# Kernel optimization log

Measured on AMD Instinct MI355X. Metric: run time of the kernel, lower is better.

Reference implementation:

```python
import jax, jax.numpy as jnp
import numpy as np

EPS = 1e-5

def setup_inputs() -> dict:
    key = jax.random.key(0)
    ks = jax.random.split(key, 6)
    N, E, C, H, L = 50000, 800000, 128, 128, 3
    x = jax.random.normal(ks[0], (N, C), dtype=jnp.float32)
    edge_index = jax.random.randint(ks[1], (2, E), 0, N, dtype=jnp.int64)
    # Xavier-ish scaled weights; layer 0 uses in=C=H so all layers stack uniformly.
    Wl = jax.random.normal(ks[2], (L, C, H), dtype=jnp.float32) / np.sqrt(C)
    Wr = jax.random.normal(ks[3], (L, C, H), dtype=jnp.float32) / np.sqrt(C)
    b = jnp.zeros((L, H), dtype=jnp.float32)
    gamma = jnp.ones((L, H), dtype=jnp.float32)
    beta = jnp.zeros((L, H), dtype=jnp.float32)
    return {"x": x, "edge_index": edge_index, "Wl": Wl, "Wr": Wr, "b": b,
            "gamma": gamma, "beta": beta}

def _sage_bn_relu(x, src, dst, Wl, Wr, b, gamma, beta):
    N = x.shape[0]
    # mean aggregation of source features into target nodes (PyG SAGEConv default)
    agg = jax.ops.segment_sum(x[src], dst, num_segments=N)          # [N, C]
    deg = jax.ops.segment_sum(jnp.ones_like(dst, dtype=x.dtype), dst, num_segments=N)
    mean_nbr = agg / jnp.maximum(deg, 1.0)[:, None]
    h = mean_nbr @ Wl + x @ Wr + b                                   # [N, H]
    # BatchNorm1d (training-mode batch statistics over nodes)
    mu = jnp.mean(h, axis=0)
    var = jnp.var(h, axis=0)
    h = gamma * (h - mu) * jax.lax.rsqrt(var + EPS) + beta
    return jax.nn.relu(h)  # dropout omitted (deterministic reference, p->0)

def reference(x, edge_index, Wl, Wr, b, gamma, beta):
    src, dst = edge_index[0], edge_index[1]
    h = x
    for l in range(Wl.shape[0]):
        h = _sage_bn_relu(h, src, dst, Wl[l], Wr[l], b[l], gamma[l], beta[l])
    return h
```

## Files before the change

kernel.cpp:

```cpp
#include <hip/hip_runtime.h>
#include <hip/hip_bf16.h>

#define BN_EPS 1e-5f
#define NPASS 4
#define NKEY 512
#define BCAP2 6144

typedef unsigned short u16;
typedef unsigned int u32;
typedef __attribute__((ext_vector_type(8))) short bf16x8v;
typedef __attribute__((ext_vector_type(4))) float f32x4v;

__device__ __forceinline__ float bf2f(u16 u){
    union { u32 i; float f; } c; c.i = ((u32)u) << 16; return c.f;
}
__device__ __forceinline__ u16 f2bf(float f){
    union { float f; u32 i; } c; c.f = f;
    u32 x = c.i;
    u32 r = x + 0x7FFFu + ((x >> 16) & 1u);
    return (u16)(r >> 16);
}
__device__ __forceinline__ float lo16(u32 u){
    union { u32 i; float f; } c; c.i = u << 16; return c.f;
}
__device__ __forceinline__ float hi16(u32 u){
    union { u32 i; float f; } c; c.i = u & 0xFFFF0000u; return c.f;
}
__device__ __forceinline__ u32 pack2(float f0, float f1){
    return (u32)f2bf(f0) | ((u32)f2bf(f1) << 16);
}

__global__ void detect_k(const int* __restrict__ ei, const u16* __restrict__ xu,
                         int* __restrict__ flags){
    int lane = threadIdx.x;
    unsigned long long bal = __ballot(ei[2 * lane + 1] != 0);
    int cnt = 0;
    #pragma unroll
    for (int k = 0; k < 4; ++k){
        u16 u = xu[2 * (lane + 64 * k)];
        int e = (u >> 7) & 0xFF;
        cnt += (e >= 0x70 && e <= 0x86) ? 1 : 0;
    }
    #pragma unroll
    for (int off = 1; off < 64; off <<= 1) cnt += __shfl_xor(cnt, off);
    if (lane == 0){
        flags[0] = (bal == 0ULL) ? 1 : 0;
        flags[1] = (cnt >= 128) ? 1 : 0;
    }
}

__global__ void prep_k(const void* __restrict__ x, const void* __restrict__ Wl,
                       const void* __restrict__ Wr, const void* __restrict__ b,
                       const void* __restrict__ g, const void* __restrict__ be,
                       u16* __restrict__ xb, u16* __restrict__ wT, float* __restrict__ p,
                       int total4, int wtot, int per, const int* __restrict__ flags){
    int i = blockIdx.x * blockDim.x + threadIdx.x;
    int bf = flags[1];
    if (i < total4){
        if (bf){
            ((uint2*)xb)[i] = ((const uint2*)x)[i];
        } else {
            float4 v = ((const float4*)x)[i];
            ushort4 o; o.x = f2bf(v.x); o.y = f2bf(v.y); o.z = f2bf(v.z); o.w = f2bf(v.w);
            ((ushort4*)xb)[i] = o;
        }
    }
    if (i < wtot){
        u16 vl = bf ? ((const u16*)Wl)[i] : f2bf(((const float*)Wl)[i]);
        u16 vr = bf ? ((const u16*)Wr)[i] : f2bf(((const float*)Wr)[i]);
        int l = i >> 14, r = (i >> 7) & 127, c = i & 127;
        wT[(size_t)(l * 2 + 0) * 16384 + c * 128 + r] = vl;
        wT[(size_t)(l * 2 + 1) * 16384 + c * 128 + r] = vr;
    }
    if (i < per){
        if (bf){
            p[i]           = bf2f(((const u16*)b)[i]);
            p[per + i]     = bf2f(((const u16*)g)[i]);
            p[2 * per + i] = bf2f(((const u16*)be)[i]);
        } else {
            p[i]           = ((const float*)b)[i];
            p[per + i]     = ((const float*)g)[i];
            p[2 * per + i] = ((const float*)be)[i];
        }
    }
}

__global__ __launch_bounds__(1024) void phist_k(const void* __restrict__ ei, int E,
                                                int tile, u32* __restrict__ blockHist,
                                                const int* __restrict__ flags){
    __shared__ u32 lh[NKEY];
    int tid = threadIdx.x;
    if (tid < NKEY) lh[tid] = 0u;
    __syncthreads();
    int start = blockIdx.x * tile;
    int end = min(E, start + tile);
    int i64 = flags[0];
    for (int i = start + tid; i < end; i += 1024){
        int s, d;
        if (i64){
            const long long* p = (const long long*)ei;
            s = (int)p[i]; d = (int)p[E + i];
        } else {
            const int* p = (const int*)ei;
            s = p[i]; d = p[E + i];
        }
        int key = ((s >> 14) << 7) | (d >> 9);
        atomicAdd(&lh[key], 1u);
    }
    __syncthreads();
    if (tid < NKEY) blockHist[blockIdx.x * NKEY + tid] = lh[tid];
}

__global__ __launch_bounds__(512) void bases_k(const u32* __restrict__ blockHist,
                                               u32* __restrict__ blockBase,
                                               int* __restrict__ rangeBase,
                                               int* __restrict__ rp2N, int nb){
    __shared__ u32 t_s[NKEY];
    int k = threadIdx.x;
    u32 run = 0;
    #pragma unroll 8
    for (int b = 0; b < nb; ++b){
        blockBase[b * NKEY + k] = run;
        run += blockHist[b * NKEY + k];
    }
    t_s[k] = min(run, (u32)BCAP2);
    __syncthreads();
    if (k == 0){
        u32 r = 0;
        for (int j = 0; j < NKEY; ++j){ u32 v = t_s[j]; t_s[j] = r; r += v; }
        rangeBase[NKEY] = (int)r;
        *rp2N = (int)r;
    }
    __syncthreads();
    rangeBase[k] = (int)t_s[k];
}

__global__ __launch_bounds__(1024) void pscat_k(const void* __restrict__ ei, int E,
                                                int tile, const u32* __restrict__ blockBase,
                                                u32* __restrict__ part,
                                                const int* __restrict__ flags){
    __shared__ u32 lcur[NKEY];
    int tid = threadIdx.x;
    if (tid < NKEY) lcur[tid] = blockBase[blockIdx.x * NKEY + tid];
    __syncthreads();
    int start = blockIdx.x * tile;
    int end = min(E, start + tile);
    int i64 = flags[0];
    for (int i = start + tid; i < end; i += 1024){
        int s, d;
        if (i64){
            const long long* p = (const long long*)ei;
            s = (int)p[i]; d = (int)p[E + i];
        } else {
            const int* p = (const int*)ei;
            s = p[i]; d = p[E + i];
        }
        int key = ((s >> 14) << 7) | (d >> 9);
        u32 pos = atomicAdd(&lcur[key], 1u);
        if (pos < BCAP2) part[(size_t)key * BCAP2 + pos] = (u32)(u16)s | ((u32)(d & 511) << 16);
    }
}

__global__ __launch_bounds__(1024) void build_k(const u32* __restrict__ part,
                                                const int* __restrict__ rangeBase,
                                                int* __restrict__ rowptr2,
                                                u16* __restrict__ col, int N){
    __shared__ u32 bins[512];
    __shared__ u32 wsum[8];
    __shared__ u16 sorted[BCAP2];
    int key  = blockIdx.x;
    int tid  = threadIdx.x;
    int base = rangeBase[key];
    int cntk = rangeBase[key + 1] - base;
    int p    = key >> 7;
    int d0   = (key & 127) << 9;
    if (tid < 512) bins[tid] = 0u;
    __syncthreads();
    const u32* pk = part + (size_t)key * BCAP2;
    for (int i = tid; i < cntk; i += 1024)
        atomicAdd(&bins[pk[i] >> 16], 1u);
    __syncthreads();
    int lane = tid & 63, w = tid >> 6;
    u32 v = (tid < 512) ? bins[tid] : 0u;
    u32 sc = v;
    #pragma unroll
    for (int off = 1; off < 64; off <<= 1){
        u32 u = __shfl_up(sc, off);
        if (lane >= off) sc += u;
    }
    if (lane == 63 && w < 8) wsum[w] = sc;
    __syncthreads();
    if (tid == 0){
        u32 r = 0;
        #pragma unroll
        for (int j = 0; j < 8; ++j){ u32 t = wsum[j]; wsum[j] = r; r += t; }
    }
    __syncthreads();
    u32 excl = (w < 8 ? wsum[w] : 0u) + sc - v;
    if (tid < 512){
        int d = d0 + tid;
        if (d < N) rowptr2[(size_t)p * N + d] = base + (int)excl;
        bins[tid] = excl;
    }
    __syncthreads();
    for (int i = tid; i < cntk; i += 1024){
        u32 e = pk[i];
        u32 pos = atomicAdd(&bins[e >> 16], 1u);
        sorted[pos] = (u16)e;
    }
    __syncthreads();
    for (int i = tid; i < cntk; i += 1024)
        col[base + i] = sorted[i];
}

#define ACC8(A, G) \
    A[0] += lo16(G.x); A[1] += hi16(G.x); \
    A[2] += lo16(G.y); A[3] += hi16(G.y); \
    A[4] += lo16(G.z); A[5] += hi16(G.z); \
    A[6] += lo16(G.w); A[7] += hi16(G.w);

__global__ __launch_bounds__(256) void agg_k(const u16* __restrict__ h,
                                             const int* __restrict__ rp2,
                                             const u16* __restrict__ col,
                                             u16* __restrict__ meanb, int N){
    int tid  = threadIdx.x;
    int gwid = (blockIdx.x * 256 + tid) >> 6;
    int lane = tid & 63;
    int quad = lane >> 4;
    int sub  = lane & 15;
    if (gwid * 8 >= N) return;
    int d0 = gwid * 8 + quad * 2;
    int d1 = d0 + 1;

    float a0[8] = {0.f,0.f,0.f,0.f,0.f,0.f,0.f,0.f};
    float a1[8] = {0.f,0.f,0.f,0.f,0.f,0.f,0.f,0.f};
    int g0 = 0, g1 = 0;

    for (int p = 0; p < NPASS; ++p){
        const int* rp = rp2 + (size_t)p * N;
        int s0 = 0, e0 = 0, s1 = 0, e1 = 0;
        if (d0 < N){ s0 = rp[d0]; e0 = rp[d0 + 1]; }
        if (d1 < N){ s1 = rp[d1]; e1 = rp[d1 + 1]; }
        g0 += e0 - s0; g1 += e1 - s1;
        int i0 = s0, i1 = s1;
        for (; i0 + 1 < e0 && i1 + 1 < e1; i0 += 2, i1 += 2){
            int sa = col[i0], sb = col[i0 + 1], sc = col[i1], sd = col[i1 + 1];
            uint4 ga = *(const uint4*)(h + (size_t)sa * 128 + sub * 8);
            uint4 gb = *(const uint4*)(h + (size_t)sb * 128 + sub * 8);
            uint4 gc = *(const uint4*)(h + (size_t)sc * 128 + sub * 8);
            uint4 gd = *(const uint4*)(h + (size_t)sd * 128 + sub * 8);
            ACC8(a0, ga); ACC8(a0, gb);
            ACC8(a1, gc); ACC8(a1, gd);
        }
        for (; i0 + 1 < e0; i0 += 2){
            int sa = col[i0], sb = col[i0 + 1];
            uint4 ga = *(const uint4*)(h + (size_t)sa * 128 + sub * 8);
            uint4 gb = *(const uint4*)(h + (size_t)sb * 128 + sub * 8);
            ACC8(a0, ga); ACC8(a0, gb);
        }
        if (i0 < e0){
            int sa = col[i0];
            uint4 ga = *(const uint4*)(h + (size_t)sa * 128 + sub * 8);
            ACC8(a0, ga);
        }
        for (; i1 + 1 < e1; i1 += 2){
            int sc = col[i1], sd = col[i1 + 1];
            uint4 gc = *(const uint4*)(h + (size_t)sc * 128 + sub * 8);
            uint4 gd = *(const uint4*)(h + (size_t)sd * 128 + sub * 8);
            ACC8(a1, gc); ACC8(a1, gd);
        }
        if (i1 < e1){
            int sc = col[i1];
            uint4 gc = *(const uint4*)(h + (size_t)sc * 128 + sub * 8);
            ACC8(a1, gc);
        }
    }

    if (d0 < N){
        float di = 1.f / fmaxf((float)g0, 1.f);
        uint4 o;
        o.x = pack2(a0[0] * di, a0[1] * di);
        o.y = pack2(a0[2] * di, a0[3] * di);
        o.z = pack2(a0[4] * di, a0[5] * di);
        o.w = pack2(a0[6] * di, a0[7] * di);
        *(uint4*)(meanb + (size_t)d0 * 128 + sub * 8) = o;
    }
    if (d1 < N){
        float di = 1.f / fmaxf((float)g1, 1.f);
        uint4 o;
        o.x = pack2(a1[0] * di, a1[1] * di);
        o.y = pack2(a1[2] * di, a1[3] * di);
        o.z = pack2(a1[4] * di, a1[5] * di);
        o.w = pack2(a1[6] * di, a1[7] * di);
        *(uint4*)(meanb + (size_t)d1 * 128 + sub * 8) = o;
    }
}
#undef ACC8

__global__ __launch_bounds__(256, 2) void gemm_k(
        const u16* __restrict__ Aa, const u16* __restrict__ Ab,
        const u16* __restrict__ wT, const float* __restrict__ bias,
        float* __restrict__ stats, u16* __restrict__ hp16, int N, int NT){
    __shared__ __align__(16) u16 sA[16384];
    int tid  = threadIdx.x;
    int lane = tid & 63;
    int w    = tid >> 6;
    int hl   = lane & 15;
    int quad = lane >> 4;
    int c0   = (2 * w)     * 16 + hl;
    int c1   = (2 * w + 1) * 16 + hl;

    bf16x8v Bf[2][2][4];
    {
        const u16* bp = wT + (size_t)(2 * w) * 2048 + (size_t)hl * 128 + quad * 8;
        #pragma unroll
        for (int tl = 0; tl < 2; ++tl)
            #pragma unroll
            for (int half = 0; half < 2; ++half)
                #pragma unroll
                for (int kc = 0; kc < 4; ++kc)
                    Bf[tl][half][kc] =
                        *(const bf16x8v*)(bp + tl * 2048 + half * 16384 + kc * 32);
    }
    float bv0 = bias[c0], bv1 = bias[c1];
    float cs0 = 0.f, cq0 = 0.f, cs1 = 0.f, cq1 = 0.f;

    int smat[4], srow[4], ssub[4], sldo[4];
    #pragma unroll
    for (int i = 0; i < 4; ++i){
        int kk  = w * 4 + i;
        int off = (kk & 7) * 1024 + lane * 16;
        int mat = kk >> 3;
        int row = off >> 8;
        int sub = (off >> 4) & 15;
        smat[i] = mat; srow[i] = row; ssub[i] = sub;
        sldo[i] = mat * 4096 + row * 128 + ((sub ^ (row & 7)) * 8);
    }
    uint4 rg0, rg1, rg2, rg3;

#define STAGE_REGS(T) { \
    int m0_ = (T) * 32; \
    int rb0_ = m0_;      if (rb0_ + 16 > N) rb0_ = N - 16; \
    int rb1_ = m0_ + 16; if (rb1_ + 16 > N) rb1_ = N - 16; \
    _Pragma("unroll") \
    for (int i_ = 0; i_ < 4; ++i_){ \
        int row_  = srow[i_]; \
        int grow_ = (row_ < 16) ? (rb0_ + row_) : (rb1_ + row_ - 16); \
        const u16* src_ = (smat[i_] ? Ab : Aa) + (size_t)grow_ * 128 + ssub[i_] * 8; \
        uint4 v_ = *(const uint4*)src_; \
        if (i_ == 0) rg0 = v_; else if (i_ == 1) rg1 = v_; \
        else if (i_ == 2) rg2 = v_; else rg3 = v_; \
    } }

#define STAGE_WRITE(B) { \
    u16* bb_ = sA + (B) * 8192; \
    *(uint4*)(bb_ + sldo[0]) = rg0; \
    *(uint4*)(bb_ + sldo[1]) = rg1; \
    *(uint4*)(bb_ + sldo[2]) = rg2; \
    *(uint4*)(bb_ + sldo[3]) = rg3; }

#define COMPUTE(B, T) { \
    int m0_ = (T) * 32; \
    int rb0_ = m0_;      bool v0_ = (m0_ + 16 <= N); if (!v0_) rb0_ = N - 16; \
    int rb1_ = m0_ + 16; bool v1_ = (m0_ + 32 <= N); if (!v1_) rb1_ = N - 16; \
    const u16* base_ = sA + (B) * 8192; \
    bf16x8v Af[2][2][4];    \
    _Pragma("unroll") \
    for (int kc_ = 0; kc_ < 4; ++kc_){ \
        int sl_ = ((quad + kc_ * 4) ^ (hl & 7)) * 8; \
        Af[0][0][kc_] = *(const bf16x8v*)(base_ +        hl * 128        + sl_); \
        Af[1][0][kc_] = *(const bf16x8v*)(base_ + (16 + hl) * 128        + sl_); \
        Af[0][1][kc_] = *(const bf16x8v*)(base_ + 4096 +        hl * 128 + sl_); \
        Af[1][1][kc_] = *(const bf16x8v*)(base_ + 4096 + (16 + hl) * 128 + sl_); \
    } \
    f32x4v acc0_[2], acc1_[2]; \
    acc0_[0] = (f32x4v){0.f,0.f,0.f,0.f}; acc0_[1] = (f32x4v){0.f,0.f,0.f,0.f}; \
    acc1_[0] = (f32x4v){0.f,0.f,0.f,0.f}; acc1_[1] = (f32x4v){0.f,0.f,0.f,0.f}; \
    _Pragma("unroll") \
    for (int half_ = 0; half_ < 2; ++half_) \
        _Pragma("unroll") \
        for (int kc_ = 0; kc_ < 4; ++kc_) \
            _Pragma("unroll") \
            for (int tl_ = 0; tl_ < 2; ++tl_){ \
                acc0_[tl_] = __builtin_amdgcn_mfma_f32_16x16x32_bf16( \
                    Af[0][half_][kc_], Bf[tl_][half_][kc_], acc0_[tl_], 0, 0, 0); \
                acc1_[tl_] = __builtin_amdgcn_mfma_f32_16x16x32_bf16( \
                    Af[1][half_][kc_], Bf[tl_][half_][kc_], acc1_[tl_], 0, 0, 0); \
            } \
    _Pragma("unroll") \
    for (int tl_ = 0; tl_ < 2; ++tl_){ \
        int   c_  = tl_ ? c1 : c0; \
        float bv_ = tl_ ? bv1 : bv0; \
        if (v0_){ \
            _Pragma("unroll") \
            for (int r_ = 0; r_ < 4; ++r_){ \
                float vv_ = acc0_[tl_][r_] + bv_; \
                hp16[(size_t)(rb0_ + quad * 4 + r_) * 128 + c_] = f2bf(vv_); \
                if (tl_){ cs1 += vv_; cq1 += vv_ * vv_; } else { cs0 += vv_; cq0 += vv_ * vv_; } \
            } \
        } \
        if (v1_){ \
            _Pragma("unroll") \
            for (int r_ = 0; r_ < 4; ++r_){ \
                float vv_ = acc1_[tl_][r_] + bv_; \
                hp16[(size_t)(rb1_ + quad * 4 + r_) * 128 + c_] = f2bf(vv_); \
                if (tl_){ cs1 += vv_; cq1 += vv_ * vv_; } else { cs0 += vv_; cq0 += vv_ * vv_; } \
            } \
        } \
    } }

    int t = blockIdx.x;
    int G = gridDim.x;
    int cur = 0;
    STAGE_REGS(t);
    STAGE_WRITE(0);
    __syncthreads();
    for (;;){
        int tn = t + G;
        bool hN = (tn < NT);
        if (hN) STAGE_REGS(tn);
        COMPUTE(cur, t);
        if (!hN) break;
        STAGE_WRITE(cur ^ 1);
        __syncthreads();
        cur ^= 1;
        t = tn;
    }
#undef STAGE_REGS
#undef STAGE_WRITE
#undef COMPUTE

    cs0 += __shfl_xor(cs0, 16); cs0 += __shfl_xor(cs0, 32);
    cq0 += __shfl_xor(cq0, 16); cq0 += __shfl_xor(cq0, 32);
    cs1 += __shfl_xor(cs1, 16); cs1 += __shfl_xor(cs1, 32);
    cq1 += __shfl_xor(cq1, 16); cq1 += __shfl_xor(cq1, 32);
    if (quad == 0){
        float* st = stats + (size_t)(blockIdx.x & 63) * 256;
        atomicAdd(&st[c0],       cs0);
        atomicAdd(&st[128 + c0], cq0);
        atomicAdd(&st[c1],       cs1);
        atomicAdd(&st[128 + c1], cq1);
    }
}

__global__ __launch_bounds__(256) void apply_k(
        const u16* __restrict__ in, const float* __restrict__ stats,
        const float* __restrict__ g, const float* __restrict__ be,
        u16* __restrict__ outb, float* __restrict__ outf, int use_f32,
        int total4, float invN){
    __shared__ float s_red[256];
    __shared__ float s_ss[256];
    int tid = threadIdx.x;
    float s = 0.f;
    #pragma unroll 8
    for (int bkt = 0; bkt < 64; ++bkt) s += stats[bkt * 256 + tid];
    s_red[tid] = s;
    __syncthreads();
    if (tid < 128){
        float mu  = s_red[tid] * invN;
        float var = s_red[128 + tid] * invN - mu * mu;
        if (!(mu == mu)) mu = 0.f;
        if (!(var >= 0.f) || !(var == var)) var = 0.f;
        float sc = g[tid] * rsqrtf(var + BN_EPS);
        s_ss[tid]       = sc;
        s_ss[128 + tid] = be[tid] - mu * sc;
    }
    __syncthreads();
    int c = (tid & 31) * 4;
    float sc0 = s_ss[c],     sh0 = s_ss[128 + c];
    float sc1 = s_ss[c + 1], sh1 = s_ss[129 + c];
    float sc2 = s_ss[c + 2], sh2 = s_ss[130 + c];
    float sc3 = s_ss[c + 3], sh3 = s_ss[131 + c];
    for (int i = blockIdx.x * blockDim.x + tid; i < total4; i += blockDim.x * gridDim.x){
        uint2 u = ((const uint2*)in)[i];
        float4 v;
        v.x = lo16(u.x); v.y = hi16(u.x); v.z = lo16(u.y); v.w = hi16(u.y);
        if (!(v.x == v.x)) v.x = 0.f;
        if (!(v.y == v.y)) v.y = 0.f;
        if (!(v.z == v.z)) v.z = 0.f;
        if (!(v.w == v.w)) v.w = 0.f;
        float r0 = fmaxf(v.x * sc0 + sh0, 0.f);
        float r1 = fmaxf(v.y * sc1 + sh1, 0.f);
        float r2 = fmaxf(v.z * sc2 + sh2, 0.f);
        float r3 = fmaxf(v.w * sc3 + sh3, 0.f);
        if (use_f32){
            float4 o; o.x = r0; o.y = r1; o.z = r2; o.w = r3;
            ((float4*)outf)[i] = o;
        } else {
            uint2 o; o.x = pack2(r0, r1); o.y = pack2(r2, r3);
            ((uint2*)outb)[i] = o;
        }
    }
}

extern "C" void kernel_launch(void* const* d_in, const int* in_sizes, int n_in,
                              void* d_out, int out_size, void* d_ws, size_t ws_size,
                              hipStream_t stream){
    const void* x  = d_in[0];
    const int*  ei = (const int*)d_in[1];
    const void* Wl = d_in[2];
    const void* Wr = d_in[3];
    const void* b  = d_in[4];
    const void* gm = d_in[5];
    const void* bt = d_in[6];
    float* outf = (float*)d_out;

    const int N = in_sizes[0] / 128;
    const int E = in_sizes[1] / 2;
    const int L = in_sizes[2] / 16384;
    const int PB = 128;
    const int TILE = (E + PB - 1) / PB;

    char* wsp = (char*)d_ws;
    size_t off = 0;
    auto alloc = [&](size_t bytes) -> char* {
        char* p = wsp + off;
        off = (off + bytes + 255) & ~(size_t)255;
        return p;
    };
    int*   flags  = (int*)  alloc(16);
    int*   rowptr2= (int*)  alloc(((size_t)NPASS * N + 1) * 4);
    u16*   col    = (u16*)  alloc((size_t)E * 2);
    u32*   bHist  = (u32*)  alloc((size_t)PB * NKEY * 4);
    u32*   bBase  = (u32*)  alloc((size_t)PB * NKEY * 4);
    int*   rangeB = (int*)  alloc((size_t)(NKEY + 1) * 4);
    u32*   part   = (u32*)  alloc((size_t)NKEY * BCAP2 * 4);
    u16*   wT     = (u16*)  alloc((size_t)L * 2 * 16384 * 2);
    float* pvec   = (float*)alloc((size_t)3 * L * 128 * 4);
    float* stats  = (float*)alloc((size_t)L * 64 * 256 * 4);
    u16*   xb     = (u16*)  alloc((size_t)N * 128 * 2);
    u16*   meanb  = (u16*)  alloc((size_t)N * 128 * 2);
    u16*   hpre16 = (u16*)  alloc((size_t)N * 128 * 2);
    u16*   hA     = (u16*)  alloc((size_t)N * 128 * 2);
    u16*   hB     = (u16*)  alloc((size_t)N * 128 * 2);
    (void)ws_size; (void)n_in; (void)out_size;

    detect_k<<<1, 64, 0, stream>>>(ei, (const u16*)x, flags);
    hipMemsetAsync(stats, 0, (size_t)L * 64 * 256 * 4, stream);

    phist_k<<<PB, 1024, 0, stream>>>((const void*)ei, E, TILE, bHist, flags);
    bases_k<<<1, 512, 0, stream>>>(bHist, bBase, rangeB, rowptr2 + (size_t)NPASS * N, PB);
    pscat_k<<<PB, 1024, 0, stream>>>((const void*)ei, E, TILE, bBase, part, flags);
    build_k<<<NKEY, 1024, 0, stream>>>(part, rangeB, rowptr2, col, N);

    prep_k<<<(N * 32 + 255) / 256, 256, 0, stream>>>(x, Wl, Wr, b, gm, bt, xb, wT, pvec,
                                                     N * 32, L * 16384, L * 128, flags);

    const u16* state = xb;
    int NT      = (N + 31) / 32;
    int gblocks = (NT + 2) / 3;
    int nwaves  = (N + 7) / 8;
    int ablocks = (nwaves + 3) / 4;
    float invN  = 1.f / (float)N;
    for (int l = 0; l < L; ++l){
        int last = (l == L - 1);
        u16* nxt = (l & 1) ? hB : hA;
        agg_k<<<ablocks, 256, 0, stream>>>(state, rowptr2, col, meanb, N);
        gemm_k<<<gblocks, 256, 0, stream>>>(meanb, state, wT + (size_t)l * 2 * 16384,
                                            pvec + (size_t)l * 128,
                                            stats + (size_t)l * 64 * 256,
                                            hpre16, N, NT);
        apply_k<<<1024, 256, 0, stream>>>(hpre16, stats + (size_t)l * 64 * 256,
                                          pvec + (size_t)L * 128 + l * 128,
                                          pvec + (size_t)2 * L * 128 + l * 128,
                                          nxt, outf, last, N * 32, invN);
        state = nxt;
    }
}
```

Before: 283.1 us.

## Fuse detect, prep and histogram kernels; unroll aggregation gather by three

```diff
diff --git a/kernel.cpp b/kernel.cpp
--- a/kernel.cpp
+++ b/kernel.cpp
@@ -30,85 +30,87 @@
     return (u32)f2bf(f0) | ((u32)f2bf(f1) << 16);
 }
 
-__global__ void detect_k(const int* __restrict__ ei, const u16* __restrict__ xu,
-                         int* __restrict__ flags){
-    int lane = threadIdx.x;
-    unsigned long long bal = __ballot(ei[2 * lane + 1] != 0);
-    int cnt = 0;
-    #pragma unroll
-    for (int k = 0; k < 4; ++k){
-        u16 u = xu[2 * (lane + 64 * k)];
-        int e = (u >> 7) & 0xFF;
-        cnt += (e >= 0x70 && e <= 0x86) ? 1 : 0;
-    }
-    #pragma unroll
-    for (int off = 1; off < 64; off <<= 1) cnt += __shfl_xor(cnt, off);
-    if (lane == 0){
-        flags[0] = (bal == 0ULL) ? 1 : 0;
-        flags[1] = (cnt >= 128) ? 1 : 0;
-    }
-}
-
-__global__ void prep_k(const void* __restrict__ x, const void* __restrict__ Wl,
-                       const void* __restrict__ Wr, const void* __restrict__ b,
-                       const void* __restrict__ g, const void* __restrict__ be,
-                       u16* __restrict__ xb, u16* __restrict__ wT, float* __restrict__ p,
-                       int total4, int wtot, int per, const int* __restrict__ flags){
-    int i = blockIdx.x * blockDim.x + threadIdx.x;
-    int bf = flags[1];
-    if (i < total4){
-        if (bf){
-            ((uint2*)xb)[i] = ((const uint2*)x)[i];
-        } else {
-            float4 v = ((const float4*)x)[i];
-            ushort4 o; o.x = f2bf(v.x); o.y = f2bf(v.y); o.z = f2bf(v.z); o.w = f2bf(v.w);
-            ((ushort4*)xb)[i] = o;
-        }
-    }
-    if (i < wtot){
-        u16 vl = bf ? ((const u16*)Wl)[i] : f2bf(((const float*)Wl)[i]);
-        u16 vr = bf ? ((const u16*)Wr)[i] : f2bf(((const float*)Wr)[i]);
-        int l = i >> 14, r = (i >> 7) & 127, c = i & 127;
-        wT[(size_t)(l * 2 + 0) * 16384 + c * 128 + r] = vl;
-        wT[(size_t)(l * 2 + 1) * 16384 + c * 128 + r] = vr;
-    }
-    if (i < per){
-        if (bf){
-            p[i]           = bf2f(((const u16*)b)[i]);
-            p[per + i]     = bf2f(((const u16*)g)[i]);
-            p[2 * per + i] = bf2f(((const u16*)be)[i]);
-        } else {
-            p[i]           = ((const float*)b)[i];
-            p[per + i]     = ((const float*)g)[i];
-            p[2 * per + i] = ((const float*)be)[i];
-        }
-    }
-}
-
-__global__ __launch_bounds__(1024) void phist_k(const void* __restrict__ ei, int E,
-                                                int tile, u32* __restrict__ blockHist,
-                                                const int* __restrict__ flags){
-    __shared__ u32 lh[NKEY];
+__global__ __launch_bounds__(1024) void prep_phist_k(
+        const void* __restrict__ x, const void* __restrict__ Wl,
+        const void* __restrict__ Wr, const void* __restrict__ b,
+        const void* __restrict__ g, const void* __restrict__ be,
+        u16* __restrict__ xb, u16* __restrict__ wT, float* __restrict__ p,
+        int total4, int wtot, int per,
+        const void* __restrict__ ei, int E, int tile, u32* __restrict__ blockHist,
+        int PB){
     int tid = threadIdx.x;
-    if (tid < NKEY) lh[tid] = 0u;
-    __syncthreads();
-    int start = blockIdx.x * tile;
-    int end = min(E, start + tile);
-    int i64 = flags[0];
-    for (int i = start + tid; i < end; i += 1024){
-        int s, d;
-        if (i64){
-            const long long* p = (const long long*)ei;
-            s = (int)p[i]; d = (int)p[E + i];
-        } else {
-            const int* p = (const int*)ei;
-            s = p[i]; d = p[E + i];
-        }
-        int key = ((s >> 14) << 7) | (d >> 9);
-        atomicAdd(&lh[key], 1u);
-    }
-    __syncthreads();
-    if (tid < NKEY) blockHist[blockIdx.x * NKEY + tid] = lh[tid];
+    if ((int)blockIdx.x < PB){
+        __shared__ u32 lh[NKEY];
+        __shared__ int s_i64;
+        if (tid < NKEY) lh[tid] = 0u;
+        if (tid < 64){
+            unsigned long long bal = __ballot(((const int*)ei)[2 * tid + 1] != 0);
+            if (tid == 0) s_i64 = (bal == 0ULL) ? 1 : 0;
+        }
+        __syncthreads();
+        int i64 = s_i64;
+        int start = blockIdx.x * tile;
+        int end = min(E, start + tile);
+        for (int i = start + tid; i < end; i += 1024){
+            int s, d;
+            if (i64){
+                const long long* pe = (const long long*)ei;
+                s = (int)pe[i]; d = (int)pe[E + i];
+            } else {
+                const int* pe = (const int*)ei;
+                s = pe[i]; d = pe[E + i];
+            }
+            int key = ((s >> 14) << 7) | (d >> 9);
+            atomicAdd(&lh[key], 1u);
+        }
+        __syncthreads();
+        if (tid < NKEY) blockHist[blockIdx.x * NKEY + tid] = lh[tid];
+    } else {
+        __shared__ int s_bf;
+        if (tid < 64){
+            const u16* xu = (const u16*)x;
+            int cnt = 0;
+            #pragma unroll
+            for (int k = 0; k < 4; ++k){
+                u16 u = xu[2 * (tid + 64 * k)];
+                int e = (u >> 7) & 0xFF;
+                cnt += (e >= 0x70 && e <= 0x86) ? 1 : 0;
+            }
+            #pragma unroll
+            for (int off = 1; off < 64; off <<= 1) cnt += __shfl_xor(cnt, off);
+            if (tid == 0) s_bf = (cnt >= 128) ? 1 : 0;
+        }
+        __syncthreads();
+        int bf = s_bf;
+        int i = ((int)blockIdx.x - PB) * 1024 + tid;
+        if (i < total4){
+            if (bf){
+                ((uint2*)xb)[i] = ((const uint2*)x)[i];
+            } else {
+                float4 v = ((const float4*)x)[i];
+                ushort4 o; o.x = f2bf(v.x); o.y = f2bf(v.y); o.z = f2bf(v.z); o.w = f2bf(v.w);
+                ((ushort4*)xb)[i] = o;
+            }
+        }
+        if (i < wtot){
+            u16 vl = bf ? ((const u16*)Wl)[i] : f2bf(((const float*)Wl)[i]);
+            u16 vr = bf ? ((const u16*)Wr)[i] : f2bf(((const float*)Wr)[i]);
+            int l = i >> 14, r = (i >> 7) & 127, c = i & 127;
+            wT[(size_t)(l * 2 + 0) * 16384 + c * 128 + r] = vl;
+            wT[(size_t)(l * 2 + 1) * 16384 + c * 128 + r] = vr;
+        }
+        if (i < per){
+            if (bf){
+                p[i]           = bf2f(((const u16*)b)[i]);
+                p[per + i]     = bf2f(((const u16*)g)[i]);
+                p[2 * per + i] = bf2f(((const u16*)be)[i]);
+            } else {
+                p[i]           = ((const float*)b)[i];
+                p[per + i]     = ((const float*)g)[i];
+                p[2 * per + i] = ((const float*)be)[i];
+            }
+        }
+    }
 }
 
 __global__ __launch_bounds__(512) void bases_k(const u32* __restrict__ blockHist,
@@ -137,15 +139,19 @@
 
 __global__ __launch_bounds__(1024) void pscat_k(const void* __restrict__ ei, int E,
                                                 int tile, const u32* __restrict__ blockBase,
-                                                u32* __restrict__ part,
-                                                const int* __restrict__ flags){
+                                                u32* __restrict__ part){
     __shared__ u32 lcur[NKEY];
+    __shared__ int s_i64;
     int tid = threadIdx.x;
     if (tid < NKEY) lcur[tid] = blockBase[blockIdx.x * NKEY + tid];
-    __syncthreads();
+    if (tid < 64){
+        unsigned long long bal = __ballot(((const int*)ei)[2 * tid + 1] != 0);
+        if (tid == 0) s_i64 = (bal == 0ULL) ? 1 : 0;
+    }
+    __syncthreads();
+    int i64 = s_i64;
     int start = blockIdx.x * tile;
     int end = min(E, start + tile);
-    int i64 = flags[0];
     for (int i = start + tid; i < end; i += 1024){
         int s, d;
         if (i64){
@@ -243,35 +249,47 @@
         if (d1 < N){ s1 = rp[d1]; e1 = rp[d1 + 1]; }
         g0 += e0 - s0; g1 += e1 - s1;
         int i0 = s0, i1 = s1;
+        for (; i0 + 2 < e0 && i1 + 2 < e1; i0 += 3, i1 += 3){
+            int na = col[i0], nb = col[i0 + 1], nc = col[i0 + 2];
+            int nd = col[i1], ne = col[i1 + 1], nf = col[i1 + 2];
+            uint4 ga = *(const uint4*)(h + (size_t)na * 128 + sub * 8);
+            uint4 gb = *(const uint4*)(h + (size_t)nb * 128 + sub * 8);
+            uint4 gc = *(const uint4*)(h + (size_t)nc * 128 + sub * 8);
+            uint4 gd = *(const uint4*)(h + (size_t)nd * 128 + sub * 8);
+            uint4 ge = *(const uint4*)(h + (size_t)ne * 128 + sub * 8);
+            uint4 gf = *(const uint4*)(h + (size_t)nf * 128 + sub * 8);
+            ACC8(a0, ga); ACC8(a0, gb); ACC8(a0, gc);
+            ACC8(a1, gd); ACC8(a1, ge); ACC8(a1, gf);
+        }
         for (; i0 + 1 < e0 && i1 + 1 < e1; i0 += 2, i1 += 2){
-            int sa = col[i0], sb = col[i0 + 1], sc = col[i1], sd = col[i1 + 1];
-            uint4 ga = *(const uint4*)(h + (size_t)sa * 128 + sub * 8);
-            uint4 gb = *(const uint4*)(h + (size_t)sb * 128 + sub * 8);
-            uint4 gc = *(const uint4*)(h + (size_t)sc * 128 + sub * 8);
-            uint4 gd = *(const uint4*)(h + (size_t)sd * 128 + sub * 8);
+            int na = col[i0], nb = col[i0 + 1], nc = col[i1], nd = col[i1 + 1];
+            uint4 ga = *(const uint4*)(h + (size_t)na * 128 + sub * 8);
+            uint4 gb = *(const uint4*)(h + (size_t)nb * 128 + sub * 8);
+            uint4 gc = *(const uint4*)(h + (size_t)nc * 128 + sub * 8);
+            uint4 gd = *(const uint4*)(h + (size_t)nd * 128 + sub * 8);
             ACC8(a0, ga); ACC8(a0, gb);
             ACC8(a1, gc); ACC8(a1, gd);
         }
         for (; i0 + 1 < e0; i0 += 2){
-            int sa = col[i0], sb = col[i0 + 1];
-            uint4 ga = *(const uint4*)(h + (size_t)sa * 128 + sub * 8);
-            uint4 gb = *(const uint4*)(h + (size_t)sb * 128 + sub * 8);
+            int na = col[i0], nb = col[i0 + 1];
+            uint4 ga = *(const uint4*)(h + (size_t)na * 128 + sub * 8);
+            uint4 gb = *(const uint4*)(h + (size_t)nb * 128 + sub * 8);
             ACC8(a0, ga); ACC8(a0, gb);
         }
         if (i0 < e0){
-            int sa = col[i0];
-            uint4 ga = *(const uint4*)(h + (size_t)sa * 128 + sub * 8);
+            int na = col[i0];
+            uint4 ga = *(const uint4*)(h + (size_t)na * 128 + sub * 8);
             ACC8(a0, ga);
         }
         for (; i1 + 1 < e1; i1 += 2){
-            int sc = col[i1], sd = col[i1 + 1];
-            uint4 gc = *(const uint4*)(h + (size_t)sc * 128 + sub * 8);
-            uint4 gd = *(const uint4*)(h + (size_t)sd * 128 + sub * 8);
+            int nc = col[i1], nd = col[i1 + 1];
+            uint4 gc = *(const uint4*)(h + (size_t)nc * 128 + sub * 8);
+            uint4 gd = *(const uint4*)(h + (size_t)nd * 128 + sub * 8);
             ACC8(a1, gc); ACC8(a1, gd);
         }
         if (i1 < e1){
-            int sc = col[i1];
-            uint4 gc = *(const uint4*)(h + (size_t)sc * 128 + sub * 8);
+            int nc = col[i1];
+            uint4 gc = *(const uint4*)(h + (size_t)nc * 128 + sub * 8);
             ACC8(a1, gc);
         }
     }
@@ -518,7 +536,6 @@
         off = (off + bytes + 255) & ~(size_t)255;
         return p;
     };
-    int*   flags  = (int*)  alloc(16);
     int*   rowptr2= (int*)  alloc(((size_t)NPASS * N + 1) * 4);
     u16*   col    = (u16*)  alloc((size_t)E * 2);
     u32*   bHist  = (u32*)  alloc((size_t)PB * NKEY * 4);
@@ -535,16 +552,16 @@
     u16*   hB     = (u16*)  alloc((size_t)N * 128 * 2);
     (void)ws_size; (void)n_in; (void)out_size;
 
-    detect_k<<<1, 64, 0, stream>>>(ei, (const u16*)x, flags);
     hipMemsetAsync(stats, 0, (size_t)L * 64 * 256 * 4, stream);
 
-    phist_k<<<PB, 1024, 0, stream>>>((const void*)ei, E, TILE, bHist, flags);
+    int prepBlocks = (N * 32 + 1023) / 1024;
+    prep_phist_k<<<PB + prepBlocks, 1024, 0, stream>>>(
+        x, Wl, Wr, b, gm, bt, xb, wT, pvec,
+        N * 32, L * 16384, L * 128,
+        (const void*)ei, E, TILE, bHist, PB);
     bases_k<<<1, 512, 0, stream>>>(bHist, bBase, rangeB, rowptr2 + (size_t)NPASS * N, PB);
-    pscat_k<<<PB, 1024, 0, stream>>>((const void*)ei, E, TILE, bBase, part, flags);
+    pscat_k<<<PB, 1024, 0, stream>>>((const void*)ei, E, TILE, bBase, part);
     build_k<<<NKEY, 1024, 0, stream>>>(part, rangeB, rowptr2, col, N);
-
-    prep_k<<<(N * 32 + 255) / 256, 256, 0, stream>>>(x, Wl, Wr, b, gm, bt, xb, wT, pvec,
-                                                     N * 32, L * 16384, L * 128, flags);
 
     const u16* state = xb;
     int NT      = (N + 31) / 32;
```

Result: slower. 289.0 us (+2.1%).
